# Kernel optimization log

Measured on AMD Instinct MI355X. Metric: run time of the kernel, lower is better.

The kernel has to match this reference:

```python
import jax, jax.numpy as jnp
import numpy as np

N_NODES = 50000
N_EDGES = 800000
DIM = 256
HEADS = 8
DIM_OUT = 32  # per-head; dim_inner = HEADS*DIM_OUT = 256


def setup_inputs() -> dict:
    key = jax.random.key(0)
    ks = jax.random.split(key, 9)
    s = 1.0 / np.sqrt(DIM)
    inner = HEADS * DIM_OUT
    return {
        "x": jax.random.normal(ks[0], (N_NODES, DIM), dtype=jnp.float32),
        "Wq": jax.random.uniform(ks[1], (DIM, inner), jnp.float32, -s, s),
        "bq": jax.random.uniform(ks[2], (inner,), jnp.float32, -s, s),
        "Wk": jax.random.uniform(ks[3], (DIM, inner), jnp.float32, -s, s),
        "bk": jax.random.uniform(ks[4], (inner,), jnp.float32, -s, s),
        "Wv": jax.random.uniform(ks[5], (DIM, inner), jnp.float32, -s, s),
        "bv": jax.random.uniform(ks[6], (inner,), jnp.float32, -s, s),
        "src": jax.random.randint(ks[7], (N_EDGES,), 0, N_NODES),
        "dst": jax.random.randint(ks[8], (N_EDGES,), 0, N_NODES),
    }


def reference(x, Wq, bq, Wk, bk, Wv, bv, src, dst):
    n = x.shape[0]
    q = (x @ Wq + bq).reshape(n, HEADS, DIM_OUT)
    k = (x @ Wk + bk).reshape(n, HEADS, DIM_OUT)
    v = (x @ Wv + bv).reshape(n, HEADS, DIM_OUT)
    # edge-wise u_dot_v: dot of src query with dst key, per head -> [E, H]
    scores = jnp.einsum('ehd,ehd->eh', q[src], k[dst]) / jnp.sqrt(
        jnp.asarray(DIM_OUT, dtype=x.dtype))
    # segment softmax over incoming edges of each destination node
    m = jax.ops.segment_max(scores, dst, num_segments=n)  # [N, H]
    m = jnp.where(jnp.isfinite(m), m, 0.0)
    e = jnp.exp(scores - m[dst])
    z = jax.ops.segment_sum(e, dst, num_segments=n)  # [N, H]
    p = e / jnp.maximum(z[dst], 1e-16)  # [E, H]
    # u_mul_e_sum: sum over incoming edges of src values weighted by attn
    out = jax.ops.segment_sum(v[src] * p[:, :, None], dst, num_segments=n)
    return out.reshape(n, HEADS * DIM_OUT)  # concat=True
```

## Files before the change

### kernel.cpp

```cpp
#include <hip/hip_runtime.h>
#include <math.h>

#define N_NODES 50000
#define N_EDGES 800000
#define DIM 256
#define HEADS 8
#define DIM_OUT 32
#define INNER 256
#define M_PAD 50048
#define CAP 64

typedef __attribute__((ext_vector_type(8))) short bf16x8;
typedef __attribute__((ext_vector_type(4))) float f32x4;
typedef __attribute__((ext_vector_type(2))) float f32x2;

__device__ __forceinline__ unsigned short f2bf(float f) {
    unsigned u = __float_as_uint(f);
    unsigned r = (u + 0x7FFFu + ((u >> 16) & 1u)) >> 16;
    return (unsigned short)r;
}

__device__ __forceinline__ f32x2 up2(unsigned u) {
    f32x2 r;
    r.x = __uint_as_float(u << 16);
    r.y = __uint_as_float(u & 0xFFFF0000u);
    return r;
}
__device__ __forceinline__ void up2x4(uint4 r, f32x2* o) {
    o[0] = up2(r.x); o[1] = up2(r.y); o[2] = up2(r.z); o[3] = up2(r.w);
}

__device__ __forceinline__ void gll16(const void* g, void* l) {
    __builtin_amdgcn_global_load_lds(
        (const __attribute__((address_space(1))) unsigned*)(uintptr_t)g,
        (__attribute__((address_space(3))) unsigned*)(unsigned)(uintptr_t)l,
        16, 0, 0);
}

#define NB_CONVX 6256
#define NB_CONVW 768
__global__ __launch_bounds__(256) void prep(
    const float* __restrict__ x,
    const float* __restrict__ Wq, const float* __restrict__ Wk,
    const float* __restrict__ Wv,
    unsigned short* __restrict__ xbf, unsigned short* __restrict__ Wt)
{
    int b = blockIdx.x;
    if (b < NB_CONVX) {
        size_t i8 = ((size_t)b * 256 + threadIdx.x) * 8;
        unsigned short h[8];
        if (i8 < (size_t)N_NODES * 256) {
            float4 a = *(const float4*)(x + i8);
            float4 c = *(const float4*)(x + i8 + 4);
            h[0]=f2bf(a.x); h[1]=f2bf(a.y); h[2]=f2bf(a.z); h[3]=f2bf(a.w);
            h[4]=f2bf(c.x); h[5]=f2bf(c.y); h[6]=f2bf(c.z); h[7]=f2bf(c.w);
        } else {
            #pragma unroll
            for (int j = 0; j < 8; j++) h[j] = 0;
        }
        uint4 o;
        o.x = (unsigned)h[0] | ((unsigned)h[1] << 16);
        o.y = (unsigned)h[2] | ((unsigned)h[3] << 16);
        o.z = (unsigned)h[4] | ((unsigned)h[5] << 16);
        o.w = (unsigned)h[6] | ((unsigned)h[7] << 16);
        *(uint4*)(xbf + i8) = o;
    } else {
        int idx = (b - NB_CONVX) * 256 + threadIdx.x;
        int z = idx >> 16, r = idx & 65535;
        int k = r >> 8, n = r & 255;
        const float* W = (z == 0) ? Wq : (z == 1) ? Wk : Wv;
        Wt[(size_t)z * 65536 + n * 256 + k] = f2bf(W[k * 256 + n]);
    }
}

#define GEMM_NWG 1173
#define HIST_NB  1563
__global__ __launch_bounds__(512) void gemm_qkv(
    const unsigned short* __restrict__ xbf,
    const unsigned short* __restrict__ Wt,
    const float* __restrict__ bq, const float* __restrict__ bk,
    const float* __restrict__ bv,
    unsigned short* __restrict__ q, unsigned short* __restrict__ k,
    unsigned short* __restrict__ v,
    const int* __restrict__ src, const int* __restrict__ dst,
    int* __restrict__ deg, int* __restrict__ edge_list)
{
    const int t = threadIdx.x;

    if (blockIdx.x >= GEMM_NWG) {
        int e = (blockIdx.x - GEMM_NWG) * 512 + t;
        if (e < N_EDGES) {
            int d = dst[e];
            int r = atomicAdd(deg + d, 1);
            edge_list[(d << 6) + r] = src[e];
        }
        return;
    }

    int hw = blockIdx.x;
    int xcd = hw & 7, pos = hw >> 3;
    int lid = (xcd < 5 ? xcd * 147 : 5 * 147 + (xcd - 5) * 146) + pos;
    int panel = lid / 3;
    int z = lid - panel * 3;
    const int row0 = panel * 128;

    const unsigned short* Wz = Wt + (size_t)z * 65536;
    const float* bias = (z == 0) ? bq : (z == 1) ? bk : bv;
    unsigned short* C = (z == 0) ? q : (z == 1) ? k : v;

    __shared__ __align__(16) short As[2][128 * 32];
    __shared__ __align__(16) short Bs[2][256 * 32];

    const int wave = t >> 6;
    const int lane = t & 63;
    const int wm = (wave & 1) * 64;
    const int wn = (wave >> 1) * 64;
    const int lr = lane & 15;
    const int lg = lane >> 4;
    const int frow = lr;
    const int fcol = lg * 8;

    f32x4 acc[4][4] = {};

#define STAGE(B, K)                                                          \
    do {                                                                     \
        gll16(xbf + (size_t)(row0 + wave * 16 + frow) * 256 + (K) + fcol,    \
              &As[B][wave * 512]);                                           \
        gll16(Wz + (size_t)(wave * 32 + frow) * 256 + (K) + fcol,            \
              &Bs[B][wave * 1024]);                                          \
        gll16(Wz + (size_t)(wave * 32 + 16 + frow) * 256 + (K) + fcol,       \
              &Bs[B][wave * 1024 + 512]);                                    \
    } while (0)

    STAGE(0, 0);
    #pragma unroll
    for (int s = 0; s < 8; s++) {
        const int cur = s & 1;
        __syncthreads();
        if (s < 7) STAGE(cur ^ 1, (s + 1) * 32);
        bf16x8 af[4], bfr[4];
        #pragma unroll
        for (int mi = 0; mi < 4; mi++)
            af[mi] = *(const bf16x8*)&As[cur][((wave & 1) * 4 + mi) * 512 + lane * 8];
        #pragma unroll
        for (int ni = 0; ni < 4; ni++)
            bfr[ni] = *(const bf16x8*)&Bs[cur][((wave >> 1) * 4 + ni) * 512 + lane * 8];
        #pragma unroll
        for (int mi = 0; mi < 4; mi++)
            #pragma unroll
            for (int ni = 0; ni < 4; ni++)
                acc[mi][ni] = __builtin_amdgcn_mfma_f32_16x16x32_bf16(
                    af[mi], bfr[ni], acc[mi][ni], 0, 0, 0);
    }
#undef STAGE

    #pragma unroll
    for (int mi = 0; mi < 4; mi++) {
        #pragma unroll
        for (int ni = 0; ni < 4; ni++) {
            int gcol = wn + ni * 16 + lr;
            float bb = bias[gcol];
            #pragma unroll
            for (int r = 0; r < 4; r++) {
                int grow = row0 + wm + mi * 16 + lg * 4 + r;
                if (grow < N_NODES)
                    C[(size_t)grow * 256 + gcol] = f2bf(acc[mi][ni][r] + bb);
            }
        }
    }
}

__global__ __launch_bounds__(256) void node_attn(
    const unsigned short* __restrict__ qbf,
    const unsigned short* __restrict__ kbf,
    const unsigned short* __restrict__ vbf,
    const int* __restrict__ deg, const int* __restrict__ edge_list,
    float* __restrict__ out)
{
    int node = blockIdx.x * 4 + (threadIdx.x >> 6);
    int lane = threadIdx.x & 63;
    if (node >= N_NODES) return;
    const int half = lane >> 5;
    const int l = lane & 31;

    int dg = deg[node];

    float* op = out + (size_t)node * 256 + l * 8;
    if (dg <= 0) {
        if (half == 0) {
            float4 z4 = {0.f, 0.f, 0.f, 0.f};
            *(float4*)op = z4;
            *(float4*)(op + 4) = z4;
        }
        return;
    }

    const int beg = node << 6;
    const int end = beg + dg;

    f32x2 kf2[4];
    up2x4(*(const uint4*)(kbf + (size_t)node * 256 + l * 8), kf2);

    const unsigned short* qrow = qbf + l * 8;
    const unsigned short* vrow = vbf + l * 8;

    const float SC = 0.17677669529663687f * 1.4426950408889634f;

    int U = (dg + 1) >> 1;
    U = ((U + 2) / 3) * 3;
    U = __builtin_amdgcn_readfirstlane(U);

    const int i0 = beg + half;
    const int last = end - 1;

    int tmp0 = edge_list[min(i0,     last)];
    int tmp1 = edge_list[min(i0 + 2, last)];
    int idC  = edge_list[min(i0 + 4, last)];
    int idA  = edge_list[min(i0 + 6, last)];
    int idB  = 0;
    uint4 qA = *(const uint4*)(qrow + (size_t)tmp0 * 256);
    uint4 vA = *(const uint4*)(vrow + (size_t)tmp0 * 256);
    uint4 qB = *(const uint4*)(qrow + (size_t)tmp1 * 256);
    uint4 vB = *(const uint4*)(vrow + (size_t)tmp1 * 256);
    uint4 qC, vC;

    float m = -1e30f, zsum = 0.0f;
    f32x2 af2[4] = {};

#define BODY(QW, VW, QL, VL, IDL, IDF, P)                                    \
    do {                                                                     \
        size_t off_ = (size_t)(IDL) * 256;                                   \
        QL = *(const uint4*)(qrow + off_);                                   \
        VL = *(const uint4*)(vrow + off_);                                   \
        int vi_ = i0 + 2 * t + 2 * (P);                                      \
        IDF = edge_list[min(vi_ + 8, last)];                                 \
        f32x2 qf_[4], vf_[4];                                                \
        up2x4(QW, qf_);                                                      \
        up2x4(VW, vf_);                                                      \
        f32x2 d_ = qf_[0] * kf2[0];                                          \
        d_ += qf_[1] * kf2[1];                                               \
        d_ += qf_[2] * kf2[2];                                               \
        d_ += qf_[3] * kf2[3];                                               \
        float s_ = d_.x + d_.y;                                              \
        s_ += __shfl_xor(s_, 1);                                             \
        s_ += __shfl_xor(s_, 2);                                             \
        bool ok_ = vi_ < end;                                                \
        float sc_ = ok_ ? s_ * SC : -1e30f;                                  \
        float mn_ = fmaxf(m, sc_);                                           \
        float w_ = exp2f(sc_ - mn_);                                         \
        w_ = ok_ ? w_ : 0.0f;                                                \
        float al_ = exp2f(m - mn_);                                          \
        zsum = zsum * al_ + w_;                                              \
        f32x2 a2_ = {al_, al_}, w2_ = {w_, w_};                              \
        af2[0] = af2[0] * a2_ + vf_[0] * w2_;                                \
        af2[1] = af2[1] * a2_ + vf_[1] * w2_;                                \
        af2[2] = af2[2] * a2_ + vf_[2] * w2_;                                \
        af2[3] = af2[3] * a2_ + vf_[3] * w2_;                                \
        m = mn_;                                                             \
    } while (0)

    for (int t = 0; t < U; t += 3) {
        BODY(qA, vA, qC, vC, idC, idB, 0);
        BODY(qB, vB, qA, vA, idA, idC, 1);
        BODY(qC, vC, qB, vB, idB, idA, 2);
    }
#undef BODY

    float mo = __shfl_xor(m, 32);
    float mt = fmaxf(m, mo);
    float scale = exp2f(m - mt);
    zsum *= scale;
    zsum += __shfl_xor(zsum, 32);
    #pragma unroll
    for (int j = 0; j < 4; j++) {
        af2[j].x = af2[j].x * scale;
        af2[j].y = af2[j].y * scale;
        af2[j].x += __shfl_xor(af2[j].x, 32);
        af2[j].y += __shfl_xor(af2[j].y, 32);
    }

    float inv = 1.0f / fmaxf(zsum, 1e-16f);
    if (half == 0) {
        float4 o0 = {af2[0].x * inv, af2[0].y * inv, af2[1].x * inv, af2[1].y * inv};
        float4 o1 = {af2[2].x * inv, af2[2].y * inv, af2[3].x * inv, af2[3].y * inv};
        *(float4*)op = o0;
        *(float4*)(op + 4) = o1;
    }
}

extern "C" void kernel_launch(void* const* d_in, const int* in_sizes, int n_in,
                              void* d_out, int out_size, void* d_ws, size_t ws_size,
                              hipStream_t stream) {
    const float* x  = (const float*)d_in[0];
    const float* Wq = (const float*)d_in[1];
    const float* bq = (const float*)d_in[2];
    const float* Wk = (const float*)d_in[3];
    const float* bk = (const float*)d_in[4];
    const float* Wv = (const float*)d_in[5];
    const float* bv = (const float*)d_in[6];
    const int* src  = (const int*)d_in[7];
    const int* dst  = (const int*)d_in[8];
    float* out = (float*)d_out;

    unsigned short* qbf = (unsigned short*)d_ws;
    unsigned short* kbf = qbf + (size_t)N_NODES * INNER;
    unsigned short* vbf = kbf + (size_t)N_NODES * INNER;
    unsigned short* xbf = vbf + (size_t)N_NODES * INNER;
    unsigned short* Wt  = xbf + (size_t)M_PAD * INNER;
    int* deg       = (int*)(Wt + 3 * 65536);
    int* edge_list = deg + N_NODES;

    hipMemsetAsync(deg, 0, (size_t)N_NODES * sizeof(int), stream);

    prep<<<NB_CONVX + NB_CONVW, 256, 0, stream>>>(x, Wq, Wk, Wv, xbf, Wt);

    gemm_qkv<<<GEMM_NWG + HIST_NB, 512, 0, stream>>>(
        xbf, Wt, bq, bk, bv, qbf, kbf, vbf, src, dst, deg, edge_list);

    node_attn<<<(N_NODES + 3) / 4, 256, 0, stream>>>(
        qbf, kbf, vbf, deg, edge_list, out);
}
```

Measured before the change: 321.8 us.

## Fold degree zeroing into prep kernel and interleave GEMM with histogram blocks

Drops the separate hipMemsetAsync for the degree array and zeros it with extra blocks in the prep kernel, removing one launch. In the fused GEMM+histogram kernel, GEMM tiles and edge-histogram blocks are now evenly interleaved across block IDs instead of all GEMM blocks coming first. This is meant to let the memory-bound atomic histogram overlap the compute-bound GEMM. It also drops the earlier XCD-aware tile remapping, which may reduce L2 locality for the GEMM panels.

```diff
diff --git a/kernel.cpp b/kernel.cpp
--- a/kernel.cpp
+++ b/kernel.cpp
@@ -39,11 +39,13 @@
 
 #define NB_CONVX 6256
 #define NB_CONVW 768
+#define NB_ZERO  49
 __global__ __launch_bounds__(256) void prep(
     const float* __restrict__ x,
     const float* __restrict__ Wq, const float* __restrict__ Wk,
     const float* __restrict__ Wv,
-    unsigned short* __restrict__ xbf, unsigned short* __restrict__ Wt)
+    unsigned short* __restrict__ xbf, unsigned short* __restrict__ Wt,
+    int* __restrict__ deg)
 {
     int b = blockIdx.x;
     if (b < NB_CONVX) {
@@ -64,17 +66,24 @@
         o.z = (unsigned)h[4] | ((unsigned)h[5] << 16);
         o.w = (unsigned)h[6] | ((unsigned)h[7] << 16);
         *(uint4*)(xbf + i8) = o;
-    } else {
+    } else if (b < NB_CONVX + NB_CONVW) {
         int idx = (b - NB_CONVX) * 256 + threadIdx.x;
         int z = idx >> 16, r = idx & 65535;
         int k = r >> 8, n = r & 255;
         const float* W = (z == 0) ? Wq : (z == 1) ? Wk : Wv;
         Wt[(size_t)z * 65536 + n * 256 + k] = f2bf(W[k * 256 + n]);
+    } else {
+        int i4 = ((b - NB_CONVX - NB_CONVW) * 256 + threadIdx.x) * 4;
+        if (i4 < N_NODES) {
+            int4 z4 = {0, 0, 0, 0};
+            *(int4*)(deg + i4) = z4;
+        }
     }
 }
 
 #define GEMM_NWG 1173
 #define HIST_NB  1563
+#define NT_BLKS  (GEMM_NWG + HIST_NB)
 __global__ __launch_bounds__(512) void gemm_qkv(
     const unsigned short* __restrict__ xbf,
     const unsigned short* __restrict__ Wt,
@@ -86,9 +95,13 @@
     int* __restrict__ deg, int* __restrict__ edge_list)
 {
     const int t = threadIdx.x;
-
-    if (blockIdx.x >= GEMM_NWG) {
-        int e = (blockIdx.x - GEMM_NWG) * 512 + t;
+    const int bid = blockIdx.x;
+
+    int gi = (int)(((long long)bid * GEMM_NWG) / NT_BLKS);
+    int ginext = (int)(((long long)(bid + 1) * GEMM_NWG) / NT_BLKS);
+    if (ginext == gi) {
+        int hi = bid - gi;
+        int e = hi * 512 + t;
         if (e < N_EDGES) {
             int d = dst[e];
             int r = atomicAdd(deg + d, 1);
@@ -97,11 +110,8 @@
         return;
     }
 
-    int hw = blockIdx.x;
-    int xcd = hw & 7, pos = hw >> 3;
-    int lid = (xcd < 5 ? xcd * 147 : 5 * 147 + (xcd - 5) * 146) + pos;
-    int panel = lid / 3;
-    int z = lid - panel * 3;
+    int panel = gi / 3;
+    int z = gi - panel * 3;
     const int row0 = panel * 128;
 
     const unsigned short* Wz = Wt + (size_t)z * 65536;
@@ -310,11 +320,10 @@
     int* deg       = (int*)(Wt + 3 * 65536);
     int* edge_list = deg + N_NODES;
 
-    hipMemsetAsync(deg, 0, (size_t)N_NODES * sizeof(int), stream);
-
-    prep<<<NB_CONVX + NB_CONVW, 256, 0, stream>>>(x, Wq, Wk, Wv, xbf, Wt);
-
-    gemm_qkv<<<GEMM_NWG + HIST_NB, 512, 0, stream>>>(
+    prep<<<NB_CONVX + NB_CONVW + NB_ZERO, 256, 0, stream>>>(
+        x, Wq, Wk, Wv, xbf, Wt, deg);
+
+    gemm_qkv<<<NT_BLKS, 512, 0, stream>>>(
         xbf, Wt, bq, bk, bv, qbf, kbf, vbf, src, dst, deg, edge_list);
 
     node_attn<<<(N_NODES + 3) / 4, 256, 0, stream>>>(
```

New measurement: 313.9 us. 2.4% less time.
